# Performance work log

Hardware: AMD Instinct MI355X
Metric: run time of the kernel (lower is better)

## Reference

```python
import jax, jax.numpy as jnp
import numpy as np

T = 8
NUM_GRAINS = 2
BETA = 10.0
TAU = 1.0
# grain assignment: T//num_grains steps per grain (remainder to early grains)
GRAIN = np.array([0, 0, 0, 0, 1, 1, 1, 1], dtype=np.int32)


@jax.custom_vjp
def heaviside_ste(x):
    # forward: hard threshold; backward: sigmoid surrogate (STE)
    return (x > 0).astype(x.dtype)

def _hs_fwd(x):
    return (x > 0).astype(x.dtype), x

def _hs_bwd(x, g):
    sig = jax.nn.sigmoid(BETA * x)
    return (g * (BETA * sig * (1.0 - sig)),)

heaviside_ste.defvjp(_hs_fwd, _hs_bwd)


def setup_inputs() -> dict:
    key = jax.random.key(0)
    x = jax.random.normal(key, (8, 2097152, 1), dtype=jnp.float32)
    d = jnp.full((NUM_GRAINS,), 2.0, dtype=jnp.float32)
    h = jnp.full((NUM_GRAINS,), 2.0, dtype=jnp.float32)
    theta = jnp.full((NUM_GRAINS,), 2.0, dtype=jnp.float32)
    return {"x": x, "d": d, "h": h, "theta": theta}


def reference(x, d, h, theta):
    g = jnp.asarray(GRAIN)                                   # [T]
    # NOTE: source always uses position_in_grain = t (grain_start stays 0)
    exps = -jnp.arange(1, T + 1, dtype=x.dtype)              # -(t+1)
    theta_t = theta[g] ** exps * TAU                         # [T]
    h_t = h[g] ** exps * TAU                                 # [T]
    d_t = d[g] ** exps * TAU                                 # [T]

    def step(v, th_ht):
        th, ht = th_ht
        s = heaviside_ste(v - th)                            # [B,N,1]
        return v - ht * s, s

    _, spikes = jax.lax.scan(step, x, (theta_t, h_t))        # [T,B,N,1]
    spikes = spikes.squeeze(-1)                              # [T,B,N]
    y = jnp.einsum('t,tbn->bn', d_t, spikes)[..., None]      # [B,N,1]
    return y
```

## Files before the change

### kernel.cpp

```cpp
#include <hip/hip_runtime.h>


#define T_STEPS 8

typedef float f32x4 __attribute__((ext_vector_type(4)));

struct Coef {
    float th[T_STEPS], hh[T_STEPS], dd[T_STEPS];
};

__device__ __forceinline__ f32x4 fs_step(const f32x4 v_in, const Coef& c) {
    f32x4 v = v_in;
    f32x4 acc = {0.0f, 0.0f, 0.0f, 0.0f};
#pragma unroll
    for (int t = 0; t < T_STEPS; ++t) {
#pragma unroll
        for (int e = 0; e < 4; ++e) {
            const float s = (v[e] > c.th[t]) ? 1.0f : 0.0f;
            v[e]   -= c.hh[t] * s;
            acc[e] += c.dd[t] * s;
        }
    }
    return acc;
}

__global__ __launch_bounds__(256) void fsneuron_kernel(
    const f32x4* __restrict__ x4,
    const float* __restrict__ d,
    const float* __restrict__ h,
    const float* __restrict__ theta,
    f32x4* __restrict__ y4,
    int n4,
    const float* __restrict__ x_tail,
    float* __restrict__ y_tail,
    int n_total)
{
    const float it0 = 1.0f / theta[0], it1 = 1.0f / theta[1];
    const float ih0 = 1.0f / h[0],     ih1 = 1.0f / h[1];
    const float id0 = 1.0f / d[0],     id1 = 1.0f / d[1];

    Coef c;
    float pt0 = 1.0f, pt1 = 1.0f, ph0 = 1.0f, ph1 = 1.0f, pd0 = 1.0f, pd1 = 1.0f;
#pragma unroll
    for (int t = 0; t < T_STEPS; ++t) {
        pt0 *= it0; pt1 *= it1;
        ph0 *= ih0; ph1 *= ih1;
        pd0 *= id0; pd1 *= id1;
        const bool g1 = (t >= 4);
        c.th[t] = g1 ? pt1 : pt0;
        c.hh[t] = g1 ? ph1 : ph0;
        c.dd[t] = g1 ? pd1 : pd0;
    }

    const int tid    = blockIdx.x * blockDim.x + threadIdx.x;
    const int stride = gridDim.x * blockDim.x;

    int i = tid;
    for (; i + stride < n4; i += 2 * stride) {
        const f32x4 va = __builtin_nontemporal_load(&x4[i]);
        const f32x4 vb = __builtin_nontemporal_load(&x4[i + stride]);
        const f32x4 ra = fs_step(va, c);
        const f32x4 rb = fs_step(vb, c);
        __builtin_nontemporal_store(ra, &y4[i]);
        __builtin_nontemporal_store(rb, &y4[i + stride]);
    }
    for (; i < n4; i += stride) {
        const f32x4 va = __builtin_nontemporal_load(&x4[i]);
        const f32x4 ra = fs_step(va, c);
        __builtin_nontemporal_store(ra, &y4[i]);
    }

    for (int j = n4 * 4 + tid; j < n_total; j += stride) {
        float v = x_tail[j];
        float acc = 0.0f;
#pragma unroll
        for (int t = 0; t < T_STEPS; ++t) {
            const float s = (v > c.th[t]) ? 1.0f : 0.0f;
            v -= c.hh[t] * s;
            acc += c.dd[t] * s;
        }
        y_tail[j] = acc;
    }
}

extern "C" void kernel_launch(void* const* d_in, const int* in_sizes, int n_in,
                              void* d_out, int out_size, void* d_ws, size_t ws_size,
                              hipStream_t stream) {
    const float* x     = (const float*)d_in[0];
    const float* d     = (const float*)d_in[1];
    const float* h     = (const float*)d_in[2];
    const float* theta = (const float*)d_in[3];
    float* y = (float*)d_out;

    const int n  = in_sizes[0];
    const int n4 = n / 4;

    const int block = 256;
    int grid = (n4 + block - 1) / block;
    if (grid > 2048) grid = 2048;
    if (grid < 1) grid = 1;

    fsneuron_kernel<<<grid, block, 0, stream>>>(
        (const f32x4*)x, d, h, theta, (f32x4*)y, n4, x, y, n);
}
```

Baseline: 27.72 us.

## Replace grid-stride loop with one-element-per-thread launch and separate tail kernel

Drops the capped 2048-block grid-stride loop with 2x unrolling and launches one thread per float4 across the full grid. The scalar tail moves into its own small kernel, launched only when n is not a multiple of four. Loads become ordinary rather than nontemporal. Each thread now recomputes the coefficient table, a small fixed cost, in exchange for more waves in flight and no loop overhead.

Result: no change. 27.66 us (-0.2%).

```diff
diff --git a/kernel.cpp b/kernel.cpp
--- a/kernel.cpp
+++ b/kernel.cpp
@@ -8,6 +8,26 @@
 struct Coef {
     float th[T_STEPS], hh[T_STEPS], dd[T_STEPS];
 };
+
+__device__ __forceinline__ void make_coef(
+    const float* __restrict__ d, const float* __restrict__ h,
+    const float* __restrict__ theta, Coef& c)
+{
+    const float it0 = 1.0f / theta[0], it1 = 1.0f / theta[1];
+    const float ih0 = 1.0f / h[0],     ih1 = 1.0f / h[1];
+    const float id0 = 1.0f / d[0],     id1 = 1.0f / d[1];
+    float pt0 = 1.0f, pt1 = 1.0f, ph0 = 1.0f, ph1 = 1.0f, pd0 = 1.0f, pd1 = 1.0f;
+#pragma unroll
+    for (int t = 0; t < T_STEPS; ++t) {
+        pt0 *= it0; pt1 *= it1;
+        ph0 *= ih0; ph1 *= ih1;
+        pd0 *= id0; pd1 *= id1;
+        const bool g1 = (t >= 4);
+        c.th[t] = g1 ? pt1 : pt0;
+        c.hh[t] = g1 ? ph1 : ph0;
+        c.dd[t] = g1 ? pd1 : pd0;
+    }
+}
 
 __device__ __forceinline__ f32x4 fs_step(const f32x4 v_in, const Coef& c) {
     f32x4 v = v_in;
@@ -30,57 +50,42 @@
     const float* __restrict__ h,
     const float* __restrict__ theta,
     f32x4* __restrict__ y4,
-    int n4,
-    const float* __restrict__ x_tail,
-    float* __restrict__ y_tail,
-    int n_total)
+    int n4)
 {
-    const float it0 = 1.0f / theta[0], it1 = 1.0f / theta[1];
-    const float ih0 = 1.0f / h[0],     ih1 = 1.0f / h[1];
-    const float id0 = 1.0f / d[0],     id1 = 1.0f / d[1];
+    const int i = blockIdx.x * blockDim.x + threadIdx.x;
+    if (i >= n4) return;
 
     Coef c;
-    float pt0 = 1.0f, pt1 = 1.0f, ph0 = 1.0f, ph1 = 1.0f, pd0 = 1.0f, pd1 = 1.0f;
+    make_coef(d, h, theta, c);
+
+    const f32x4 v = x4[i];
+    const f32x4 r = fs_step(v, c);
+    __builtin_nontemporal_store(r, &y4[i]);
+}
+
+__global__ __launch_bounds__(64) void fsneuron_tail_kernel(
+    const float* __restrict__ x,
+    const float* __restrict__ d,
+    const float* __restrict__ h,
+    const float* __restrict__ theta,
+    float* __restrict__ y,
+    int start, int n_total)
+{
+    const int i = start + blockIdx.x * blockDim.x + threadIdx.x;
+    if (i >= n_total) return;
+
+    Coef c;
+    make_coef(d, h, theta, c);
+
+    float v = x[i];
+    float acc = 0.0f;
 #pragma unroll
     for (int t = 0; t < T_STEPS; ++t) {
-        pt0 *= it0; pt1 *= it1;
-        ph0 *= ih0; ph1 *= ih1;
-        pd0 *= id0; pd1 *= id1;
-        const bool g1 = (t >= 4);
-        c.th[t] = g1 ? pt1 : pt0;
-        c.hh[t] = g1 ? ph1 : ph0;
-        c.dd[t] = g1 ? pd1 : pd0;
+        const float s = (v > c.th[t]) ? 1.0f : 0.0f;
+        v   -= c.hh[t] * s;
+        acc += c.dd[t] * s;
     }
-
-    const int tid    = blockIdx.x * blockDim.x + threadIdx.x;
-    const int stride = gridDim.x * blockDim.x;
-
-    int i = tid;
-    for (; i + stride < n4; i += 2 * stride) {
-        const f32x4 va = __builtin_nontemporal_load(&x4[i]);
-        const f32x4 vb = __builtin_nontemporal_load(&x4[i + stride]);
-        const f32x4 ra = fs_step(va, c);
-        const f32x4 rb = fs_step(vb, c);
-        __builtin_nontemporal_store(ra, &y4[i]);
-        __builtin_nontemporal_store(rb, &y4[i + stride]);
-    }
-    for (; i < n4; i += stride) {
-        const f32x4 va = __builtin_nontemporal_load(&x4[i]);
-        const f32x4 ra = fs_step(va, c);
-        __builtin_nontemporal_store(ra, &y4[i]);
-    }
-
-    for (int j = n4 * 4 + tid; j < n_total; j += stride) {
-        float v = x_tail[j];
-        float acc = 0.0f;
-#pragma unroll
-        for (int t = 0; t < T_STEPS; ++t) {
-            const float s = (v > c.th[t]) ? 1.0f : 0.0f;
-            v -= c.hh[t] * s;
-            acc += c.dd[t] * s;
-        }
-        y_tail[j] = acc;
-    }
+    y[i] = acc;
 }
 
 extern "C" void kernel_launch(void* const* d_in, const int* in_sizes, int n_in,
@@ -96,10 +101,15 @@
     const int n4 = n / 4;
 
     const int block = 256;
-    int grid = (n4 + block - 1) / block;
-    if (grid > 2048) grid = 2048;
-    if (grid < 1) grid = 1;
+    const int grid  = (n4 + block - 1) / block;
+    if (grid > 0) {
+        fsneuron_kernel<<<grid, block, 0, stream>>>(
+            (const f32x4*)x, d, h, theta, (f32x4*)y, n4);
+    }
 
-    fsneuron_kernel<<<grid, block, 0, stream>>>(
-        (const f32x4*)x, d, h, theta, (f32x4*)y, n4, x, y, n);
+    const int tail = n - n4 * 4;
+    if (tail > 0) {
+        fsneuron_tail_kernel<<<(tail + 63) / 64, 64, 0, stream>>>(
+            x, d, h, theta, y, n4 * 4, n);
+    }
 }
```
